# Kernel tuning notes

Hardware: AMD Instinct MI355X
Metric: run time of the kernel (lower is better)

Reference implementation:

```python
import jax, jax.numpy as jnp
import numpy as np

B, S, H, I, E, K = 4, 2048, 2048, 5632, 8, 2


def setup_inputs() -> dict:
    key = jax.random.key(0)
    k0, k1, k2, k3, k4 = jax.random.split(key, 5)
    std_p = 1.0 / np.sqrt(H)
    return {
        "hidden_states": jax.random.normal(k0, (B, S, H), dtype=jnp.float32),
        "router_w": jax.random.normal(k1, (E, H), dtype=jnp.float32) * 0.02,
        "w_gate": jax.random.normal(k2, (E, H, I), dtype=jnp.float32) * std_p,
        "w_up": jax.random.normal(k3, (E, H, I), dtype=jnp.float32) * std_p,
        "w_down": jax.random.normal(k4, (E, I, H), dtype=jnp.float32) * (1.0 / np.sqrt(I)),
    }


def reference(hidden_states, router_w, w_gate, w_up, w_down):
    b, s, h = hidden_states.shape
    x = hidden_states.reshape(-1, h)                       # [T, H]
    router_logits = x @ router_w.T                          # [T, E]
    routing_weights = jax.nn.softmax(router_logits, axis=-1)
    top_w, top_i = jax.lax.top_k(routing_weights, K)        # [T, K]
    top_w = top_w / jnp.sum(top_w, axis=-1, keepdims=True)  # renormalize over top-k
    # combine[t, e] = sum_k top_w[t, k] * (top_i[t, k] == e)
    combine = jnp.sum(jax.nn.one_hot(top_i, E, dtype=top_w.dtype) * top_w[..., None], axis=1)  # [T, E]
    out = jnp.zeros_like(x)
    for e in range(E):  # small fixed expert count
        # SwiGLU expert MLP: down(silu(gate(x)) * up(x))
        act = jax.nn.silu(x @ w_gate[e]) * (x @ w_up[e])    # [T, I]
        out = out + (act @ w_down[e]) * combine[:, e:e + 1]
    return (out.reshape(b, s, h),
            router_logits.reshape(b, s, E),
            top_i.reshape(b, s, K),
            top_w.reshape(b, s, K))
```

## Files before the change

kernel.cpp:

```cpp
#include <hip/hip_runtime.h>
#include <hip/hip_bf16.h>
#include <stdint.h>

#define NTOK 8192
#define HD   2048
#define ID   5632
#define NE   8
#define NASSIGN (NTOK * 2)
#define MAXT256 (NASSIGN / 256 + NE)

typedef __attribute__((ext_vector_type(8))) short  bf16x8;
typedef __attribute__((ext_vector_type(4))) float  f32x4;
typedef __attribute__((ext_vector_type(8))) unsigned short u16x8;

__device__ __forceinline__ unsigned short f2bf(float f) {
  union { float f; unsigned int u; } c; c.f = f;
  unsigned int lsb = (c.u >> 16) & 1u;
  return (unsigned short)((c.u + 0x7fffu + lsb) >> 16);
}

__device__ __forceinline__ void async16(const void* g, void* l) {
  __builtin_amdgcn_global_load_lds(
      (const __attribute__((address_space(1))) void*)g,
      (__attribute__((address_space(3))) void*)l, 16, 0, 0);
}

__global__ __launch_bounds__(256) void k_router(
    const float* __restrict__ x, const float* __restrict__ rw,
    float* __restrict__ out_logits, float* __restrict__ out_topi,
    float* __restrict__ out_topw,
    int* __restrict__ tk_e, float* __restrict__ tk_w, int* __restrict__ cnts)
{
  const int wid = threadIdx.x >> 6, lane = threadIdx.x & 63;
  const int t = blockIdx.x * 4 + wid;
  const float* xr = x + (size_t)t * HD;
  float acc[NE];
#pragma unroll
  for (int e = 0; e < NE; e++) acc[e] = 0.f;
#pragma unroll
  for (int i = 0; i < 8; i++) {
    const int col = lane * 4 + i * 256;
    const float4 xv = *(const float4*)(xr + col);
#pragma unroll
    for (int e = 0; e < NE; e++) {
      const float4 wv = *(const float4*)(rw + e * HD + col);
      acc[e] += xv.x * wv.x + xv.y * wv.y + xv.z * wv.z + xv.w * wv.w;
    }
  }
#pragma unroll
  for (int e = 0; e < NE; e++)
    for (int o = 32; o >= 1; o >>= 1) acc[e] += __shfl_xor(acc[e], o, 64);

  if (lane == 0) {
    int i1 = 0;
#pragma unroll
    for (int e = 1; e < NE; e++) if (acc[e] > acc[i1]) i1 = e;
    int i2 = (i1 == 0) ? 1 : 0;
#pragma unroll
    for (int e = 0; e < NE; e++) if (e != i1 && acc[e] > acc[i2]) i2 = e;
    float p2 = __expf(acc[i2] - acc[i1]);
    float s  = 1.f + p2;
    float w1 = 1.f / s, w2 = p2 / s;
#pragma unroll
    for (int e = 0; e < NE; e++) out_logits[(size_t)t * NE + e] = acc[e];
    out_topi[t * 2 + 0] = (float)i1; out_topi[t * 2 + 1] = (float)i2;
    out_topw[t * 2 + 0] = w1;        out_topw[t * 2 + 1] = w2;
    tk_e[t * 2 + 0] = i1; tk_e[t * 2 + 1] = i2;
    tk_w[t * 2 + 0] = w1; tk_w[t * 2 + 1] = w2;
    atomicAdd(&cnts[i1], 1); atomicAdd(&cnts[i2], 1);
  }
}

__global__ void k_scan(const int* __restrict__ cnts, int* __restrict__ offs,
                       int* __restrict__ cursor, int* __restrict__ tile_e,
                       int* __restrict__ tile_rt, int* __restrict__ ntiles) {
  if (threadIdx.x == 0) {
    int s = 0, nt = 0;
    for (int e = 0; e < NE; e++) {
      offs[e] = s; cursor[e] = s;
      int ntl = (cnts[e] + 255) >> 8;
      for (int i = 0; i < ntl; i++) { tile_e[nt] = e; tile_rt[nt] = i; nt++; }
      s += cnts[e];
    }
    ntiles[0] = nt;
  }
}

__global__ void k_assign(const int* __restrict__ tk_e, const float* __restrict__ tk_w,
                         int* __restrict__ cursor, int* __restrict__ perm,
                         float* __restrict__ pw, int* __restrict__ inv) {
  int t = blockIdx.x * 256 + threadIdx.x;
  if (t >= NTOK) return;
#pragma unroll
  for (int k = 0; k < 2; k++) {
    int e = tk_e[t * 2 + k];
    int pos = atomicAdd(&cursor[e], 1);
    perm[pos] = t;
    pw[pos] = tk_w[t * 2 + k];
    inv[t * 2 + k] = pos;
  }
}

__global__ __launch_bounds__(256) void k_gather(const float* __restrict__ x,
    const int* __restrict__ perm, unsigned short* __restrict__ xg) {
  const int r = blockIdx.x;
  const int tok = perm[r];
  const float* src = x + (size_t)tok * HD;
  unsigned short* dst = xg + (size_t)r * HD;
  const int c = threadIdx.x * 8;
  float4 a = *(const float4*)(src + c);
  float4 b = *(const float4*)(src + c + 4);
  u16x8 o;
  o[0] = f2bf(a.x); o[1] = f2bf(a.y); o[2] = f2bf(a.z); o[3] = f2bf(a.w);
  o[4] = f2bf(b.x); o[5] = f2bf(b.y); o[6] = f2bf(b.z); o[7] = f2bf(b.w);
  *(u16x8*)(dst + c) = o;
}

__global__ __launch_bounds__(256) void k_conv64(const float* __restrict__ in0,
    const float* __restrict__ in1, unsigned short* __restrict__ out0,
    unsigned short* __restrict__ out1, int R, int C, int nmat) {
  __shared__ unsigned short tlb[64][72];
  const int z = blockIdx.z;
  const int mat = (nmat == 2) ? (z & 1) : 0;
  const int e   = (nmat == 2) ? (z >> 1) : z;
  const float* in = ((mat == 0) ? in0 : in1) + (size_t)e * R * C;
  unsigned short* out = ((mat == 0) ? out0 : out1) + (size_t)e * (size_t)R * C;
  const int tid = threadIdx.x;
  const int c0 = blockIdx.x * 64, r0 = blockIdx.y * 64;
#pragma unroll
  for (int pass = 0; pass < 4; ++pass) {
    const int kr = pass * 16 + (tid >> 4);
    const int cc = (tid & 15) * 4;
    const float4 v = *(const float4*)(in + (size_t)(r0 + kr) * C + c0 + cc);
    tlb[cc + 0][kr] = f2bf(v.x); tlb[cc + 1][kr] = f2bf(v.y);
    tlb[cc + 2][kr] = f2bf(v.z); tlb[cc + 3][kr] = f2bf(v.w);
  }
  __syncthreads();
#pragma unroll
  for (int pass = 0; pass < 2; ++pass) {
    const int n = pass * 32 + (tid >> 3);
    const int k = (tid & 7) * 8;
    *(u16x8*)(out + (size_t)(c0 + n) * R + r0 + k) = *(const u16x8*)&tlb[n][k];
  }
}

#define GBUF(b) ((b) * 32768)

__global__ __launch_bounds__(512, 2) void k_gemm_gu256f(
    const unsigned short* __restrict__ A,
    const unsigned short* __restrict__ BgT, const unsigned short* __restrict__ BuT,
    const int* __restrict__ cnts, const int* __restrict__ offs,
    const int* __restrict__ tile_e, const int* __restrict__ tile_rt,
    const int* __restrict__ ntiles, unsigned short* __restrict__ gact)
{
  const int raw = blockIdx.x;
  const int v = (raw & 7) * ((int)gridDim.x >> 3) + (raw >> 3);
  const int ct = v / MAXT256;
  const int ti = v % MAXT256;
  if (ti >= ntiles[0]) return;
  const int e = tile_e[ti], rt = tile_rt[ti];
  const int cnt = cnts[e], off = offs[e];
  const int tid = threadIdx.x;

  __shared__ __align__(16) char smem[131072];

  const unsigned short* Bg = BgT + (size_t)e * (size_t)ID * HD;
  const unsigned short* Bu = BuT + (size_t)e * (size_t)ID * HD;
  const size_t arow0 = (size_t)off + (size_t)rt * 256;
  const size_t bcol0 = (size_t)ct * 128;

  const int r0s = tid >> 2;
  const int c0s = (((tid & 3) ^ ((tid >> 3) & 3)) * 8);

  const int NTS = HD / 32;

  auto STAGE_A = [&](int bb, int kt) {
    const int kc = kt * 32;
    async16(A + (arow0 + r0s) * (size_t)HD + kc + c0s, smem + GBUF(bb) + tid * 16);
    async16(A + (arow0 + 128 + r0s) * (size_t)HD + kc + c0s, smem + GBUF(bb) + 8192 + tid * 16);
  };
  auto STAGE_B = [&](int bb, int kt) {
    const int kc = kt * 32;
    async16(Bg + (bcol0 + r0s) * (size_t)HD + kc + c0s, smem + GBUF(bb) + 16384 + tid * 16);
    async16(Bu + (bcol0 + r0s) * (size_t)HD + kc + c0s, smem + GBUF(bb) + 24576 + tid * 16);
  };

  f32x4 accg[8][2], accu[8][2];
#pragma unroll
  for (int m = 0; m < 8; m++)
#pragma unroll
    for (int n = 0; n < 2; n++) { accg[m][n] = (f32x4)0.f; accu[m][n] = (f32x4)0.f; }

  const int lane = tid & 63, wid = tid >> 6;
  const int wm = wid >> 2, wn = wid & 3;
  const int fr = lane & 15;
  const int slot = ((lane >> 4) ^ ((fr >> 1) & 3));
  const int laddr = (fr << 6) + (slot << 4);

  STAGE_A(0, 0); STAGE_B(0, 0);
  STAGE_A(1, 1); STAGE_B(1, 1);
  STAGE_A(2, 2); STAGE_B(2, 2);
  asm volatile("s_waitcnt vmcnt(8)" ::: "memory");
  asm volatile("s_barrier" ::: "memory");

  bf16x8 bgr[2], bur[2];
  for (int s = 0; s < NTS; ++s) {
    const int bi = s & 3;
    char* base = smem + GBUF(bi);
    int sn = s + 3; sn = sn < NTS - 1 ? sn : NTS - 1;
    const int bn = (s + 3) & 3;
    asm volatile("s_waitcnt vmcnt(8)" ::: "memory");
    {
      bf16x8 afr[4];
#pragma unroll
      for (int t = 0; t < 4; t++)
        afr[t] = *(const bf16x8*)(base + ((wm*128 + t*16) << 6) + laddr);
#pragma unroll
      for (int t = 0; t < 2; t++) {
        bgr[t] = *(const bf16x8*)(base + 16384 + ((wn*32 + t*16) << 6) + laddr);
        bur[t] = *(const bf16x8*)(base + 24576 + ((wn*32 + t*16) << 6) + laddr);
      }
      STAGE_A(bn, sn);
      __builtin_amdgcn_s_setprio(1);
#pragma unroll
      for (int t = 0; t < 4; t++)
#pragma unroll
        for (int n = 0; n < 2; n++) {
          accg[t][n] = __builtin_amdgcn_mfma_f32_16x16x32_bf16(afr[t], bgr[n], accg[t][n], 0, 0, 0);
          accu[t][n] = __builtin_amdgcn_mfma_f32_16x16x32_bf16(afr[t], bur[n], accu[t][n], 0, 0, 0);
        }
      __builtin_amdgcn_s_setprio(0);
    }
    asm volatile("s_barrier" ::: "memory");
    {
      bf16x8 afr[4];
#pragma unroll
      for (int t = 0; t < 4; t++)
        afr[t] = *(const bf16x8*)(base + ((wm*128 + 64 + t*16) << 6) + laddr);
      STAGE_B(bn, sn);
      __builtin_amdgcn_s_setprio(1);
#pragma unroll
      for (int t = 0; t < 4; t++)
#pragma unroll
        for (int n = 0; n < 2; n++) {
          accg[4 + t][n] = __builtin_amdgcn_mfma_f32_16x16x32_bf16(afr[t], bgr[n], accg[4 + t][n], 0, 0, 0);
          accu[4 + t][n] = __builtin_amdgcn_mfma_f32_16x16x32_bf16(afr[t], bur[n], accu[4 + t][n], 0, 0, 0);
        }
      __builtin_amdgcn_s_setprio(0);
    }
    asm volatile("s_barrier" ::: "memory");
  }
  asm volatile("s_waitcnt vmcnt(0)" ::: "memory");

  const int crow = (lane >> 4) * 4, ccol = lane & 15;
  const int rbase = rt * 256 + wm * 128;
#pragma unroll
  for (int mt = 0; mt < 8; ++mt) {
#pragma unroll
    for (int j = 0; j < 4; ++j) {
      const int rl = rbase + (mt & 3) * 16 + (mt >> 2) * 64 + crow + j;
      if (rl >= cnt) continue;
      const size_t grow = (size_t)off + rl;
#pragma unroll
      for (int nt = 0; nt < 2; ++nt) {
        const int col = (int)bcol0 + wn * 32 + nt * 16 + ccol;
        const float g = accg[(mt >> 2) * 4 + (mt & 3)][nt][j];
        const float u = accu[(mt >> 2) * 4 + (mt & 3)][nt][j];
        const float a = g / (1.f + __expf(-g)) * u;
        gact[grow * (size_t)ID + col] = f2bf(a);
      }
    }
  }
}

__global__ __launch_bounds__(512, 2) void k_gemm_dn256(
    const unsigned short* __restrict__ A,
    const unsigned short* __restrict__ Wbase,
    const int* __restrict__ cnts, const int* __restrict__ offs,
    const int* __restrict__ tile_e, const int* __restrict__ tile_rt,
    const int* __restrict__ ntiles,
    const float* __restrict__ pw, float* __restrict__ dbuf)
{
  const int raw = blockIdx.x;
  const int v = (raw & 7) * ((int)gridDim.x >> 3) + (raw >> 3);
  const int ti = v % MAXT256;
  const int rest = v / MAXT256;
  const int ksplit = rest & 1;
  const int ct = rest >> 1;
  if (ti >= ntiles[0]) return;
  const int e = tile_e[ti], rt = tile_rt[ti];
  const int cnt = cnts[e], off = offs[e];
  const int tid = threadIdx.x;

  __shared__ __align__(16) char smem[131072];

  const unsigned short* W = Wbase + (size_t)e * (size_t)HD * ID;
  const size_t arow0 = (size_t)off + (size_t)rt * 256;
  const size_t bcol0 = (size_t)ct * 256;
  const int kbase = ksplit * (ID / 2);

  const int r0s = tid >> 2;
  const int c0s = (((tid & 3) ^ ((tid >> 3) & 3)) * 8);

  const int NTS = (ID / 2) / 32;

  auto STAGE_A = [&](int bb, int kt) {
    const int kc = kbase + kt * 32;
    async16(A + (arow0 + r0s) * (size_t)ID + kc + c0s, smem + GBUF(bb) + tid * 16);
    async16(A + (arow0 + 128 + r0s) * (size_t)ID + kc + c0s, smem + GBUF(bb) + 8192 + tid * 16);
  };
  auto STAGE_B = [&](int bb, int kt) {
    const int kc = kbase + kt * 32;
    async16(W + (bcol0 + r0s) * (size_t)ID + kc + c0s, smem + GBUF(bb) + 16384 + tid * 16);
    async16(W + (bcol0 + 128 + r0s) * (size_t)ID + kc + c0s, smem + GBUF(bb) + 24576 + tid * 16);
  };

  f32x4 acc[8][4];
#pragma unroll
  for (int m = 0; m < 8; m++)
#pragma unroll
    for (int n = 0; n < 4; n++) acc[m][n] = (f32x4)0.f;

  const int lane = tid & 63, wid = tid >> 6;
  const int wm = wid >> 2, wn = wid & 3;
  const int fr = lane & 15;
  const int slot = ((lane >> 4) ^ ((fr >> 1) & 3));
  const int laddr = (fr << 6) + (slot << 4);

  STAGE_A(0, 0); STAGE_B(0, 0);
  STAGE_A(1, 1); STAGE_B(1, 1);
  STAGE_A(2, 2); STAGE_B(2, 2);
  asm volatile("s_waitcnt vmcnt(8)" ::: "memory");
  asm volatile("s_barrier" ::: "memory");

  bf16x8 bfr[4];
  for (int s = 0; s < NTS; ++s) {
    const int bi = s & 3;
    char* base = smem + GBUF(bi);
    int sn = s + 3; sn = sn < NTS - 1 ? sn : NTS - 1;
    const int bn = (s + 3) & 3;
    asm volatile("s_waitcnt vmcnt(8)" ::: "memory");
    {
      bf16x8 afr[4];
#pragma unroll
      for (int t = 0; t < 4; t++)
        afr[t] = *(const bf16x8*)(base + ((wm*128 + t*16) << 6) + laddr);
#pragma unroll
      for (int t = 0; t < 4; t++)
        bfr[t] = *(const bf16x8*)(base + 16384 + ((wn*64 + t*16) << 6) + laddr);
      STAGE_A(bn, sn);
      __builtin_amdgcn_s_setprio(1);
#pragma unroll
      for (int t = 0; t < 4; t++)
#pragma unroll
        for (int n = 0; n < 4; n++)
          acc[t][n] = __builtin_amdgcn_mfma_f32_16x16x32_bf16(afr[t], bfr[n], acc[t][n], 0, 0, 0);
      __builtin_amdgcn_s_setprio(0);
    }
    asm volatile("s_barrier" ::: "memory");
    {
      bf16x8 afr[4];
#pragma unroll
      for (int t = 0; t < 4; t++)
        afr[t] = *(const bf16x8*)(base + ((wm*128 + 64 + t*16) << 6) + laddr);
      STAGE_B(bn, sn);
      __builtin_amdgcn_s_setprio(1);
#pragma unroll
      for (int t = 0; t < 4; t++)
#pragma unroll
        for (int n = 0; n < 4; n++)
          acc[4 + t][n] = __builtin_amdgcn_mfma_f32_16x16x32_bf16(afr[t], bfr[n], acc[4 + t][n], 0, 0, 0);
      __builtin_amdgcn_s_setprio(0);
    }
    asm volatile("s_barrier" ::: "memory");
  }
  asm volatile("s_waitcnt vmcnt(0)" ::: "memory");

  float* db = dbuf + (size_t)ksplit * (size_t)NASSIGN * HD;
  const int crow = (lane >> 4) * 4, ccol = lane & 15;
  const int rbase = rt * 256 + wm * 128;
#pragma unroll
  for (int mt = 0; mt < 8; ++mt) {
#pragma unroll
    for (int j = 0; j < 4; ++j) {
      const int rl = rbase + (mt & 3) * 16 + (mt >> 2) * 64 + crow + j;
      if (rl >= cnt) continue;
      const size_t grow = (size_t)off + rl;
      const float wgt = pw[grow];
#pragma unroll
      for (int nt = 0; nt < 4; ++nt) {
        const int col = (int)bcol0 + wn * 64 + nt * 16 + ccol;
        db[grow * (size_t)HD + col] = acc[(mt >> 2) * 4 + (mt & 3)][nt][j] * wgt;
      }
    }
  }
}

__global__ __launch_bounds__(256) void k_combine(const float* __restrict__ dbuf,
    const int* __restrict__ inv, float* __restrict__ out) {
  const int t = blockIdx.x;
  const int p0 = inv[t * 2], p1 = inv[t * 2 + 1];
  const float* d1 = dbuf + (size_t)NASSIGN * HD;
  const float4* a0 = (const float4*)(dbuf + (size_t)p0 * HD);
  const float4* a1 = (const float4*)(dbuf + (size_t)p1 * HD);
  const float4* b0 = (const float4*)(d1 + (size_t)p0 * HD);
  const float4* b1 = (const float4*)(d1 + (size_t)p1 * HD);
  float4* o = (float4*)(out + (size_t)t * HD);
#pragma unroll
  for (int i = 0; i < 2; i++) {
    int c = threadIdx.x + i * 256;
    float4 x0 = a0[c], x1 = a1[c], y0 = b0[c], y1 = b1[c];
    o[c] = make_float4(x0.x + x1.x + y0.x + y1.x, x0.y + x1.y + y0.y + y1.y,
                       x0.z + x1.z + y0.z + y1.z, x0.w + x1.w + y0.w + y1.w);
  }
}

extern "C" void kernel_launch(void* const* d_in, const int* in_sizes, int n_in,
                              void* d_out, int out_size, void* d_ws, size_t ws_size,
                              hipStream_t stream) {
  const float* x  = (const float*)d_in[0];
  const float* rw = (const float*)d_in[1];
  const float* wg = (const float*)d_in[2];
  const float* wu = (const float*)d_in[3];
  const float* wd = (const float*)d_in[4];

  float* outp       = (float*)d_out;
  float* out_logits = outp + (size_t)NTOK * HD;
  float* out_topi   = out_logits + (size_t)NTOK * NE;
  float* out_topw   = out_topi + (size_t)NTOK * 2;

  char* w = (char*)d_ws;
  int*   cnts    = (int*)(w + 0);
  int*   offs    = (int*)(w + 64);
  int*   cursor  = (int*)(w + 128);
  int*   ntiles  = (int*)(w + 192);
  int*   tile_e  = (int*)(w + 256);
  int*   tile_rt = (int*)(w + 1280);
  int*   tk_e    = (int*)(w + 4096);
  float* tk_w    = (float*)(w + 4096 + 65536);
  int*   perm    = (int*)(w + 4096 + 2 * 65536);
  float* pw      = (float*)(w + 4096 + 3 * 65536);
  int*   inv     = (int*)(w + 4096 + 4 * 65536);

  char* big = w + (1 << 20);
  unsigned short* xg = (unsigned short*)big;
  const size_t XG_E = (size_t)(NASSIGN + 256) * HD;
  unsigned short* wgT = xg + XG_E;
  const size_t WT_E = (size_t)NE * ID * HD;
  unsigned short* wuT  = wgT + WT_E;
  unsigned short* wdT  = wuT + WT_E;
  unsigned short* gact = wdT + WT_E;
  const size_t GA_E = (size_t)(NASSIGN + 256) * ID;
  float* dbuf = (float*)(gact + GA_E);

  hipMemsetAsync(d_ws, 0, 256, stream);

  k_conv64<<<dim3(ID / 64, HD / 64, 2 * NE), 256, 0, stream>>>(
      wg, wu, wgT, wuT, HD, ID, 2);
  k_conv64<<<dim3(HD / 64, ID / 64, NE), 256, 0, stream>>>(
      wd, nullptr, wdT, nullptr, ID, HD, 1);

  k_router<<<NTOK / 4, 256, 0, stream>>>(x, rw, out_logits, out_topi, out_topw,
                                         tk_e, tk_w, cnts);
  k_scan<<<1, 64, 0, stream>>>(cnts, offs, cursor, tile_e, tile_rt, ntiles);
  k_assign<<<NTOK / 256, 256, 0, stream>>>(tk_e, tk_w, cursor, perm, pw, inv);
  k_gather<<<NASSIGN, 256, 0, stream>>>(x, perm, xg);

  k_gemm_gu256f<<<dim3((ID / 128) * MAXT256), 512, 0, stream>>>(
      xg, wgT, wuT, cnts, offs, tile_e, tile_rt, ntiles, gact);
  k_gemm_dn256<<<dim3((HD / 256) * 2 * MAXT256), 512, 0, stream>>>(
      gact, wdT, cnts, offs, tile_e, tile_rt, ntiles, pw, dbuf);
  k_combine<<<NTOK, 256, 0, stream>>>(dbuf, inv, outp);
}
```

Baseline: 1.813 ms.

## Merge router and weight conversion into one launch; drop split-K in down GEMM

Folds the router and the three weight transpose/bf16 conversion kernels into a single launch that dispatches on block index, removing two launches and letting the router overlap with conversion. Separately, removes the 2-way K split in the down-projection GEMM, halving its grid while each block walks the full K. The combine kernel then reads one partial buffer per assignment instead of two, cutting dbuf traffic. The trade-off is a smaller down GEMM grid (fewer blocks to fill the CUs) in exchange for less fp32 write/read traffic.

```diff
diff --git a/kernel.cpp b/kernel.cpp
--- a/kernel.cpp
+++ b/kernel.cpp
@@ -9,6 +9,10 @@
 #define NASSIGN (NTOK * 2)
 #define MAXT256 (NASSIGN / 256 + NE)
 
+#define NB_ROUTER 2048
+#define NB_CONVGU (88 * 32 * 16)
+#define NB_CONVD  (32 * 88 * 8)
+
 typedef __attribute__((ext_vector_type(8))) short  bf16x8;
 typedef __attribute__((ext_vector_type(4))) float  f32x4;
 typedef __attribute__((ext_vector_type(8))) unsigned short u16x8;
@@ -25,49 +29,99 @@
       (__attribute__((address_space(3))) void*)l, 16, 0, 0);
 }
 
-__global__ __launch_bounds__(256) void k_router(
+__device__ __forceinline__ void conv_body(const float* in, unsigned short* out,
+    int R, int C, int bx, int by, unsigned short (*tlb)[72]) {
+  const int tid = threadIdx.x;
+  const int c0 = bx * 64, r0 = by * 64;
+#pragma unroll
+  for (int pass = 0; pass < 4; ++pass) {
+    const int kr = pass * 16 + (tid >> 4);
+    const int cc = (tid & 15) * 4;
+    const float4 v = *(const float4*)(in + (size_t)(r0 + kr) * C + c0 + cc);
+    tlb[cc + 0][kr] = f2bf(v.x); tlb[cc + 1][kr] = f2bf(v.y);
+    tlb[cc + 2][kr] = f2bf(v.z); tlb[cc + 3][kr] = f2bf(v.w);
+  }
+  __syncthreads();
+#pragma unroll
+  for (int pass = 0; pass < 2; ++pass) {
+    const int n = pass * 32 + (tid >> 3);
+    const int k = (tid & 7) * 8;
+    *(u16x8*)(out + (size_t)(c0 + n) * R + r0 + k) = *(const u16x8*)&tlb[n][k];
+  }
+}
+
+__global__ __launch_bounds__(256) void k_mega(
     const float* __restrict__ x, const float* __restrict__ rw,
     float* __restrict__ out_logits, float* __restrict__ out_topi,
     float* __restrict__ out_topw,
-    int* __restrict__ tk_e, float* __restrict__ tk_w, int* __restrict__ cnts)
+    int* __restrict__ tk_e, float* __restrict__ tk_w, int* __restrict__ cnts,
+    const float* __restrict__ wg, const float* __restrict__ wu,
+    const float* __restrict__ wd,
+    unsigned short* __restrict__ wgT, unsigned short* __restrict__ wuT,
+    unsigned short* __restrict__ wdT)
 {
-  const int wid = threadIdx.x >> 6, lane = threadIdx.x & 63;
-  const int t = blockIdx.x * 4 + wid;
-  const float* xr = x + (size_t)t * HD;
-  float acc[NE];
-#pragma unroll
-  for (int e = 0; e < NE; e++) acc[e] = 0.f;
-#pragma unroll
-  for (int i = 0; i < 8; i++) {
-    const int col = lane * 4 + i * 256;
-    const float4 xv = *(const float4*)(xr + col);
-#pragma unroll
-    for (int e = 0; e < NE; e++) {
-      const float4 wv = *(const float4*)(rw + e * HD + col);
-      acc[e] += xv.x * wv.x + xv.y * wv.y + xv.z * wv.z + xv.w * wv.w;
-    }
-  }
-#pragma unroll
-  for (int e = 0; e < NE; e++)
-    for (int o = 32; o >= 1; o >>= 1) acc[e] += __shfl_xor(acc[e], o, 64);
-
-  if (lane == 0) {
-    int i1 = 0;
-#pragma unroll
-    for (int e = 1; e < NE; e++) if (acc[e] > acc[i1]) i1 = e;
-    int i2 = (i1 == 0) ? 1 : 0;
-#pragma unroll
-    for (int e = 0; e < NE; e++) if (e != i1 && acc[e] > acc[i2]) i2 = e;
-    float p2 = __expf(acc[i2] - acc[i1]);
-    float s  = 1.f + p2;
-    float w1 = 1.f / s, w2 = p2 / s;
-#pragma unroll
-    for (int e = 0; e < NE; e++) out_logits[(size_t)t * NE + e] = acc[e];
-    out_topi[t * 2 + 0] = (float)i1; out_topi[t * 2 + 1] = (float)i2;
-    out_topw[t * 2 + 0] = w1;        out_topw[t * 2 + 1] = w2;
-    tk_e[t * 2 + 0] = i1; tk_e[t * 2 + 1] = i2;
-    tk_w[t * 2 + 0] = w1; tk_w[t * 2 + 1] = w2;
-    atomicAdd(&cnts[i1], 1); atomicAdd(&cnts[i2], 1);
+  __shared__ unsigned short tlb[64][72];
+  int bid = blockIdx.x;
+
+  if (bid < NB_ROUTER) {
+    const int wid = threadIdx.x >> 6, lane = threadIdx.x & 63;
+    const int t = bid * 4 + wid;
+    const float* xr = x + (size_t)t * HD;
+    float acc[NE];
+#pragma unroll
+    for (int e = 0; e < NE; e++) acc[e] = 0.f;
+#pragma unroll
+    for (int i = 0; i < 8; i++) {
+      const int col = lane * 4 + i * 256;
+      const float4 xv = *(const float4*)(xr + col);
+#pragma unroll
+      for (int e = 0; e < NE; e++) {
+        const float4 wv = *(const float4*)(rw + e * HD + col);
+        acc[e] += xv.x * wv.x + xv.y * wv.y + xv.z * wv.z + xv.w * wv.w;
+      }
+    }
+#pragma unroll
+    for (int e = 0; e < NE; e++)
+      for (int o = 32; o >= 1; o >>= 1) acc[e] += __shfl_xor(acc[e], o, 64);
+
+    if (lane == 0) {
+      int i1 = 0;
+#pragma unroll
+      for (int e = 1; e < NE; e++) if (acc[e] > acc[i1]) i1 = e;
+      int i2 = (i1 == 0) ? 1 : 0;
+#pragma unroll
+      for (int e = 0; e < NE; e++) if (e != i1 && acc[e] > acc[i2]) i2 = e;
+      float p2 = __expf(acc[i2] - acc[i1]);
+      float s  = 1.f + p2;
+      float w1 = 1.f / s, w2 = p2 / s;
+#pragma unroll
+      for (int e = 0; e < NE; e++) out_logits[(size_t)t * NE + e] = acc[e];
+      out_topi[t * 2 + 0] = (float)i1; out_topi[t * 2 + 1] = (float)i2;
+      out_topw[t * 2 + 0] = w1;        out_topw[t * 2 + 1] = w2;
+      tk_e[t * 2 + 0] = i1; tk_e[t * 2 + 1] = i2;
+      tk_w[t * 2 + 0] = w1; tk_w[t * 2 + 1] = w2;
+      atomicAdd(&cnts[i1], 1); atomicAdd(&cnts[i2], 1);
+    }
+    return;
+  }
+  bid -= NB_ROUTER;
+  if (bid < NB_CONVGU) {
+    const int z = bid / (88 * 32);
+    const int rem = bid % (88 * 32);
+    const int by = rem / 88, bx = rem % 88;
+    const int mat = z & 1, e = z >> 1;
+    const float* in = ((mat == 0) ? wg : wu) + (size_t)e * HD * ID;
+    unsigned short* out = ((mat == 0) ? wgT : wuT) + (size_t)e * (size_t)ID * HD;
+    conv_body(in, out, HD, ID, bx, by, tlb);
+    return;
+  }
+  bid -= NB_CONVGU;
+  {
+    const int z = bid / (32 * 88);
+    const int rem = bid % (32 * 88);
+    const int by = rem / 32, bx = rem % 32;
+    conv_body(wd + (size_t)z * ID * HD, wdT + (size_t)z * (size_t)HD * ID,
+              ID, HD, bx, by, tlb);
   }
 }
 
@@ -114,34 +168,6 @@
   o[0] = f2bf(a.x); o[1] = f2bf(a.y); o[2] = f2bf(a.z); o[3] = f2bf(a.w);
   o[4] = f2bf(b.x); o[5] = f2bf(b.y); o[6] = f2bf(b.z); o[7] = f2bf(b.w);
   *(u16x8*)(dst + c) = o;
-}
-
-__global__ __launch_bounds__(256) void k_conv64(const float* __restrict__ in0,
-    const float* __restrict__ in1, unsigned short* __restrict__ out0,
-    unsigned short* __restrict__ out1, int R, int C, int nmat) {
-  __shared__ unsigned short tlb[64][72];
-  const int z = blockIdx.z;
-  const int mat = (nmat == 2) ? (z & 1) : 0;
-  const int e   = (nmat == 2) ? (z >> 1) : z;
-  const float* in = ((mat == 0) ? in0 : in1) + (size_t)e * R * C;
-  unsigned short* out = ((mat == 0) ? out0 : out1) + (size_t)e * (size_t)R * C;
-  const int tid = threadIdx.x;
-  const int c0 = blockIdx.x * 64, r0 = blockIdx.y * 64;
-#pragma unroll
-  for (int pass = 0; pass < 4; ++pass) {
-    const int kr = pass * 16 + (tid >> 4);
-    const int cc = (tid & 15) * 4;
-    const float4 v = *(const float4*)(in + (size_t)(r0 + kr) * C + c0 + cc);
-    tlb[cc + 0][kr] = f2bf(v.x); tlb[cc + 1][kr] = f2bf(v.y);
-    tlb[cc + 2][kr] = f2bf(v.z); tlb[cc + 3][kr] = f2bf(v.w);
-  }
-  __syncthreads();
-#pragma unroll
-  for (int pass = 0; pass < 2; ++pass) {
-    const int n = pass * 32 + (tid >> 3);
-    const int k = (tid & 7) * 8;
-    *(u16x8*)(out + (size_t)(c0 + n) * R + r0 + k) = *(const u16x8*)&tlb[n][k];
-  }
 }
 
 #define GBUF(b) ((b) * 32768)
@@ -283,10 +309,8 @@
 {
   const int raw = blockIdx.x;
   const int v = (raw & 7) * ((int)gridDim.x >> 3) + (raw >> 3);
+  const int ct = v / MAXT256;
   const int ti = v % MAXT256;
-  const int rest = v / MAXT256;
-  const int ksplit = rest & 1;
-  const int ct = rest >> 1;
   if (ti >= ntiles[0]) return;
   const int e = tile_e[ti], rt = tile_rt[ti];
   const int cnt = cnts[e], off = offs[e];
@@ -297,20 +321,19 @@
   const unsigned short* W = Wbase + (size_t)e * (size_t)HD * ID;
   const size_t arow0 = (size_t)off + (size_t)rt * 256;
   const size_t bcol0 = (size_t)ct * 256;
-  const int kbase = ksplit * (ID / 2);
 
   const int r0s = tid >> 2;
   const int c0s = (((tid & 3) ^ ((tid >> 3) & 3)) * 8);
 
-  const int NTS = (ID / 2) / 32;
+  const int NTS = ID / 32;
 
   auto STAGE_A = [&](int bb, int kt) {
-    const int kc = kbase + kt * 32;
+    const int kc = kt * 32;
     async16(A + (arow0 + r0s) * (size_t)ID + kc + c0s, smem + GBUF(bb) + tid * 16);
     async16(A + (arow0 + 128 + r0s) * (size_t)ID + kc + c0s, smem + GBUF(bb) + 8192 + tid * 16);
   };
   auto STAGE_B = [&](int bb, int kt) {
-    const int kc = kbase + kt * 32;
+    const int kc = kt * 32;
     async16(W + (bcol0 + r0s) * (size_t)ID + kc + c0s, smem + GBUF(bb) + 16384 + tid * 16);
     async16(W + (bcol0 + 128 + r0s) * (size_t)ID + kc + c0s, smem + GBUF(bb) + 24576 + tid * 16);
   };
@@ -376,7 +399,6 @@
   }
   asm volatile("s_waitcnt vmcnt(0)" ::: "memory");
 
-  float* db = dbuf + (size_t)ksplit * (size_t)NASSIGN * HD;
   const int crow = (lane >> 4) * 4, ccol = lane & 15;
   const int rbase = rt * 256 + wm * 128;
 #pragma unroll
@@ -390,7 +412,7 @@
 #pragma unroll
       for (int nt = 0; nt < 4; ++nt) {
         const int col = (int)bcol0 + wn * 64 + nt * 16 + ccol;
-        db[grow * (size_t)HD + col] = acc[(mt >> 2) * 4 + (mt & 3)][nt][j] * wgt;
+        dbuf[grow * (size_t)HD + col] = acc[(mt >> 2) * 4 + (mt & 3)][nt][j] * wgt;
       }
     }
   }
@@ -400,18 +422,14 @@
     const int* __restrict__ inv, float* __restrict__ out) {
   const int t = blockIdx.x;
   const int p0 = inv[t * 2], p1 = inv[t * 2 + 1];
-  const float* d1 = dbuf + (size_t)NASSIGN * HD;
-  const float4* a0 = (const float4*)(dbuf + (size_t)p0 * HD);
-  const float4* a1 = (const float4*)(dbuf + (size_t)p1 * HD);
-  const float4* b0 = (const float4*)(d1 + (size_t)p0 * HD);
-  const float4* b1 = (const float4*)(d1 + (size_t)p1 * HD);
+  const float4* r0 = (const float4*)(dbuf + (size_t)p0 * HD);
+  const float4* r1 = (const float4*)(dbuf + (size_t)p1 * HD);
   float4* o = (float4*)(out + (size_t)t * HD);
 #pragma unroll
   for (int i = 0; i < 2; i++) {
     int c = threadIdx.x + i * 256;
-    float4 x0 = a0[c], x1 = a1[c], y0 = b0[c], y1 = b1[c];
-    o[c] = make_float4(x0.x + x1.x + y0.x + y1.x, x0.y + x1.y + y0.y + y1.y,
-                       x0.z + x1.z + y0.z + y1.z, x0.w + x1.w + y0.w + y1.w);
+    float4 a = r0[c], b = r1[c];
+    o[c] = make_float4(a.x + b.x, a.y + b.y, a.z + b.z, a.w + b.w);
   }
 }
 
@@ -455,20 +473,17 @@
 
   hipMemsetAsync(d_ws, 0, 256, stream);
 
-  k_conv64<<<dim3(ID / 64, HD / 64, 2 * NE), 256, 0, stream>>>(
-      wg, wu, wgT, wuT, HD, ID, 2);
-  k_conv64<<<dim3(HD / 64, ID / 64, NE), 256, 0, stream>>>(
-      wd, nullptr, wdT, nullptr, ID, HD, 1);
-
-  k_router<<<NTOK / 4, 256, 0, stream>>>(x, rw, out_logits, out_topi, out_topw,
-                                         tk_e, tk_w, cnts);
+  k_mega<<<NB_ROUTER + NB_CONVGU + NB_CONVD, 256, 0, stream>>>(
+      x, rw, out_logits, out_topi, out_topw, tk_e, tk_w, cnts,
+      wg, wu, wd, wgT, wuT, wdT);
+
   k_scan<<<1, 64, 0, stream>>>(cnts, offs, cursor, tile_e, tile_rt, ntiles);
   k_assign<<<NTOK / 256, 256, 0, stream>>>(tk_e, tk_w, cursor, perm, pw, inv);
   k_gather<<<NASSIGN, 256, 0, stream>>>(x, perm, xg);
 
   k_gemm_gu256f<<<dim3((ID / 128) * MAXT256), 512, 0, stream>>>(
       xg, wgT, wuT, cnts, offs, tile_e, tile_rt, ntiles, gact);
-  k_gemm_dn256<<<dim3((HD / 256) * 2 * MAXT256), 512, 0, stream>>>(
+  k_gemm_dn256<<<dim3((HD / 256) * MAXT256), 512, 0, stream>>>(
       gact, wdT, cnts, offs, tile_e, tile_rt, ntiles, pw, dbuf);
   k_combine<<<NTOK, 256, 0, stream>>>(dbuf, inv, outp);
 }
```

Result: faster. 1.771 ms (-2.3%).
